# Kernel optimization log

Measured on AMD Instinct MI355X. Metric: run time of the kernel, lower is better.

Reference implementation:

```python
import jax, jax.numpy as jnp
import numpy as np
from jax import lax

HIDDEN = 256
HORIZON = 168  # 7 * 24


def _cell(x, h, c, Wih, Whh, bih, bhh):
    # PyTorch LSTM cell: gate order i, f, g, o
    gates = x @ Wih.T + bih + h @ Whh.T + bhh  # [B, 4*HIDDEN]
    i, f, g, o = jnp.split(gates, 4, axis=-1)
    c = jax.nn.sigmoid(f) * c + jax.nn.sigmoid(i) * jnp.tanh(g)
    h = jax.nn.sigmoid(o) * jnp.tanh(c)
    return h, c


def setup_inputs() -> dict:
    key = jax.random.key(0)
    ks = jax.random.split(key, 20)
    B, T, H = 1024, 336, HIDDEN
    s = 0.05

    def p(k, shape):
        return jax.random.normal(k, shape, dtype=jnp.float32) * s

    inp = {"x": jax.random.normal(ks[0], (B, T), dtype=jnp.float32)}
    # encoder layer 0 (input_size=1), layer 1 (input=HIDDEN)
    inp["enc_Wih0"] = p(ks[1], (4 * H, 1)); inp["enc_Whh0"] = p(ks[2], (4 * H, H))
    inp["enc_bih0"] = p(ks[3], (4 * H,)); inp["enc_bhh0"] = p(ks[4], (4 * H,))
    inp["enc_Wih1"] = p(ks[5], (4 * H, H)); inp["enc_Whh1"] = p(ks[6], (4 * H, H))
    inp["enc_bih1"] = p(ks[7], (4 * H,)); inp["enc_bhh1"] = p(ks[8], (4 * H,))
    # decoder layers
    inp["dec_Wih0"] = p(ks[9], (4 * H, 1)); inp["dec_Whh0"] = p(ks[10], (4 * H, H))
    inp["dec_bih0"] = p(ks[11], (4 * H,)); inp["dec_bhh0"] = p(ks[12], (4 * H,))
    inp["dec_Wih1"] = p(ks[13], (4 * H, H)); inp["dec_Whh1"] = p(ks[14], (4 * H, H))
    inp["dec_bih1"] = p(ks[15], (4 * H,)); inp["dec_bhh1"] = p(ks[16], (4 * H,))
    # final projection hidden -> 1
    inp["fc_W"] = p(ks[17], (1, H)); inp["fc_b"] = p(ks[18], (1,))
    return inp


def reference(x, enc_Wih0, enc_Whh0, enc_bih0, enc_bhh0,
              enc_Wih1, enc_Whh1, enc_bih1, enc_bhh1,
              dec_Wih0, dec_Whh0, dec_bih0, dec_bhh0,
              dec_Wih1, dec_Whh1, dec_bih1, dec_bhh1,
              fc_W, fc_b):
    B = x.shape[0]
    xs = x[:, :, None].transpose(1, 0, 2)  # [T, B, 1]
    z = jnp.zeros((B, HIDDEN), dtype=x.dtype)

    def enc_step(carry, xt):
        h0, c0, h1, c1 = carry
        h0, c0 = _cell(xt, h0, c0, enc_Wih0, enc_Whh0, enc_bih0, enc_bhh0)
        h1, c1 = _cell(h0, h1, c1, enc_Wih1, enc_Whh1, enc_bih1, enc_bhh1)
        return (h0, c0, h1, c1), None

    (h0, c0, h1, c1), _ = lax.scan(enc_step, (z, z, z, z), xs)

    dec_inp = x[:, -1:]  # [B, 1] last observed value

    def dec_step(carry, _):
        h0, c0, h1, c1, inp = carry
        h0, c0 = _cell(inp, h0, c0, dec_Wih0, dec_Whh0, dec_bih0, dec_bhh0)
        h1, c1 = _cell(h0, h1, c1, dec_Wih1, dec_Whh1, dec_bih1, dec_bhh1)
        pred = h1 @ fc_W.T + fc_b  # [B, 1]
        return (h0, c0, h1, c1, pred), pred

    _, preds = lax.scan(dec_step, (h0, c0, h1, c1, dec_inp), None, length=HORIZON)
    return preds[:, :, 0].T  # [B, HORIZON]
```

## Files before the change

kernel.cpp:

```cpp
#include <hip/hip_runtime.h>

#define HIDDEN 256
#define TENC 336
#define HORIZ 168
#define BSZ 1024
#define BH (BSZ*HIDDEN)

typedef _Float16 f16;
typedef f16 f16x8 __attribute__((ext_vector_type(8)));
typedef float f32x4 __attribute__((ext_vector_type(4)));
typedef unsigned int u32;
typedef unsigned long long u64;

#define H0_OFF 0
#define H1_OFF (2*BH*2)
#define PRED_OFF (H1_OFF + 2*BH*2)
#define FLAG_OFF (PRED_OFF + 2*BSZ*4)
#define WS_TOTAL (FLAG_OFF + 256*128)

#define LDS_A0 0
#define LDS_A1 32768
#define LDS_X0 65536
#define LDS_X1 81920
#define LDS_SM 98304
#define LDS_TOTAL (LDS_SM + 1024)

__device__ __forceinline__ float sigm(float x){ return 1.0f/(1.0f+__expf(-x)); }
__device__ __forceinline__ float tanh_f(float x){ return 2.0f/(1.0f+__expf(-2.0f*x)) - 1.0f; }

__device__ __forceinline__ u64 ald64(const f16* p){
  return __hip_atomic_load((const u64*)p, __ATOMIC_RELAXED, __HIP_MEMORY_SCOPE_AGENT);
}
__device__ __forceinline__ u32 ald32(const u32* p){
  return __hip_atomic_load(p, __ATOMIC_RELAXED, __HIP_MEMORY_SCOPE_AGENT);
}
__device__ __forceinline__ float aldf(const float* p){
  return __hip_atomic_load(p, __ATOMIC_RELAXED, __HIP_MEMORY_SCOPE_AGENT);
}
__device__ __forceinline__ void ast32(u32* p, u32 v){
  __hip_atomic_store(p, v, __ATOMIC_RELAXED, __HIP_MEMORY_SCOPE_AGENT);
}
__device__ __forceinline__ void astf(float* p, float v){
  __hip_atomic_store(p, v, __ATOMIC_RELAXED, __HIP_MEMORY_SCOPE_AGENT);
}

__device__ __forceinline__ f16x8 loadWfrag(const float* W, int grow, int k){
  const float* p = W + grow*HIDDEN + k;
  float4 lo = *(const float4*)p;
  float4 hi = *(const float4*)(p+4);
  f16x8 r;
  r[0]=(f16)lo.x; r[1]=(f16)lo.y; r[2]=(f16)lo.z; r[3]=(f16)lo.w;
  r[4]=(f16)hi.x; r[5]=(f16)hi.y; r[6]=(f16)hi.z; r[7]=(f16)hi.w;
  return r;
}

__device__ __forceinline__ void stage_tile(char* dst, const f16* src_base, int g, int tid){
  #pragma unroll
  for (int i=0;i<4;++i){
    int s = tid + 512*i;
    int l = s & 63, f = s >> 6;
    int kt = f >> 2, mt = f & 3;
    int row = g*64 + mt*16 + (l&15);
    int k = kt*32 + 8*(l>>4);
    const f16* src = src_base + row*HIDDEN + k;
    u64 a = ald64(src), b = ald64(src+4);
    *(u64*)(dst + s*16) = a;
    *(u64*)(dst + s*16 + 8) = b;
  }
}

__device__ __forceinline__ void cellpair(const float* X, const float* bs, const float* wih, float xr,
                                         int crow, int dp, float& ca, float& cb, float& hA, float& hB){
  float iA = X[(0*64+crow)*16+dp  ] + bs[dp]      + xr*wih[dp];
  float iB = X[(0*64+crow)*16+dp+1] + bs[dp+1]    + xr*wih[dp+1];
  float fA = X[(1*64+crow)*16+dp  ] + bs[16+dp]   + xr*wih[16+dp];
  float fB = X[(1*64+crow)*16+dp+1] + bs[16+dp+1] + xr*wih[16+dp+1];
  float gA = X[(2*64+crow)*16+dp  ] + bs[32+dp]   + xr*wih[32+dp];
  float gB = X[(2*64+crow)*16+dp+1] + bs[32+dp+1] + xr*wih[32+dp+1];
  float oA = X[(3*64+crow)*16+dp  ] + bs[48+dp]   + xr*wih[48+dp];
  float oB = X[(3*64+crow)*16+dp+1] + bs[48+dp+1] + xr*wih[48+dp+1];
  ca = sigm(fA)*ca + sigm(iA)*tanh_f(gA);
  cb = sigm(fB)*cb + sigm(iB)*tanh_f(gB);
  hA = sigm(oA)*tanh_f(ca);
  hB = sigm(oB)*tanh_f(cb);
}

__device__ __forceinline__ void storeh(f16* base, int rowg, int col, float hA, float hB){
  u32 pk = (u32)__builtin_bit_cast(unsigned short, (f16)hA)
         | ((u32)__builtin_bit_cast(unsigned short, (f16)hB) << 16);
  __hip_atomic_store((u32*)(base + rowg*HIDDEN + col), pk, __ATOMIC_RELAXED, __HIP_MEMORY_SCOPE_AGENT);
}

__device__ __forceinline__ void gbar(u32* flags, int g, int j, int lane, int tid, u32 ev){
  __syncthreads();
  if (tid == 0) ast32(&flags[(g*16 + j)*32], ev);
  const u32* sp = &flags[(g*16 + (lane&15))*32];
  bool done = false;
  for (int it = 0; it < (1<<16) && !done; ++it){
    u32 v = ald32(sp);
    done = (__all((int)(v >= ev)) != 0);
  }
}

struct P {
  const float *x;
  const float *eWih0,*eWhh0,*eBih0,*eBhh0,*eWih1,*eWhh1,*eBih1,*eBhh1;
  const float *dWih0,*dWhh0,*dBih0,*dBhh0,*dWih1,*dWhh1,*dBih1,*dBhh1;
  const float *fcW,*fcB;
  float* out;
  char* ws;
};

__global__ void initk(char* ws){
  u32* p = (u32*)ws;
  size_t total = (size_t)WS_TOTAL / 4;
  for (size_t k = (size_t)blockIdx.x*blockDim.x + threadIdx.x; k < total;
       k += (size_t)gridDim.x*blockDim.x) p[k] = 0u;
}

__global__ __launch_bounds__(512, 2) void lstm_main(P p){
  const int tid  = threadIdx.x;
  const int lane = tid & 63;
  const int w    = tid >> 6;
  const int n    = w & 3;
  const int mh   = w >> 2;
  const int blk  = blockIdx.x;
  const int g    = blk & 15;
  const int j    = blk >> 4;

  extern __shared__ __align__(16) char smem[];
  char*  A0 = smem + LDS_A0;
  char*  A1 = smem + LDS_A1;
  float* X0 = (float*)(smem + LDS_X0);
  float* X1 = (float*)(smem + LDS_X1);
  float* wih0s = (float*)(smem + LDS_SM);
  float* b0s   = wih0s + 64;
  float* b1s   = wih0s + 128;
  float* fcWs  = wih0s + 192;
  float* fcbs  = wih0s + 208;

  f16*   h0buf = (f16*)(p.ws + H0_OFF);
  f16*   h1buf = (f16*)(p.ws + H1_OFF);
  float* predb = (float*)(p.ws + PRED_OFF);
  u32*   flags = (u32*)(p.ws + FLAG_OFF);

  const int crow = tid >> 3;
  const int dp   = (tid & 7) * 2;
  const int rowg = g*64 + crow;
  const int cold = j*16 + dp;

  float c0a=0.f, c0b=0.f, c1a=0.f, c1b=0.f;

  if (tid < 64){
    int gt = tid >> 4, d = tid & 15;
    int grow = gt*256 + j*16 + d;
    wih0s[tid] = p.eWih0[grow];
    b0s[tid] = p.eBih0[grow] + p.eBhh0[grow];
    b1s[tid] = p.eBih1[grow] + p.eBhh1[grow];
  }
  if (tid < 16) fcWs[tid] = p.fcW[j*16 + tid];
  if (tid == 0) fcbs[0] = p.fcB[0];

  f16x8 B0[8], B1i[8], B1h[8];
  {
    int grow = n*256 + j*16 + (lane & 15);
    int kb = 8*(lane>>4);
    #pragma unroll
    for (int kt=0; kt<8; ++kt){
      B0[kt]  = loadWfrag(p.eWhh0, grow, kt*32 + kb);
      B1i[kt] = loadWfrag(p.eWih1, grow, kt*32 + kb);
      B1h[kt] = loadWfrag(p.eWhh1, grow, kt*32 + kb);
    }
  }
  __syncthreads();

  u32 ev = 0;

  for (int r = 0; r <= TENC; ++r){
    stage_tile(A0, h0buf + ((r+1)&1)*BH, g, tid);
    stage_tile(A1, h1buf + (r&1)*BH,     g, tid);
    __syncthreads();

    f32x4 acc0[2] = {{0.f,0.f,0.f,0.f},{0.f,0.f,0.f,0.f}};
    f32x4 acc1[2] = {{0.f,0.f,0.f,0.f},{0.f,0.f,0.f,0.f}};
    #pragma unroll
    for (int kt=0; kt<8; ++kt){
      #pragma unroll
      for (int m=0; m<2; ++m){
        f16x8 a = *(const f16x8*)(A0 + ((kt*4 + (mh*2+m))*64 + lane)*16);
        acc0[m] = __builtin_amdgcn_mfma_f32_16x16x32_f16(a, B0[kt],  acc0[m], 0,0,0);
        acc1[m] = __builtin_amdgcn_mfma_f32_16x16x32_f16(a, B1i[kt], acc1[m], 0,0,0);
      }
    }
    #pragma unroll
    for (int kt=0; kt<8; ++kt){
      #pragma unroll
      for (int m=0; m<2; ++m){
        f16x8 a = *(const f16x8*)(A1 + ((kt*4 + (mh*2+m))*64 + lane)*16);
        acc1[m] = __builtin_amdgcn_mfma_f32_16x16x32_f16(a, B1h[kt], acc1[m], 0,0,0);
      }
    }

    #pragma unroll
    for (int m=0; m<2; ++m){
      int rb = mh*32 + m*16 + 4*(lane>>4);
      #pragma unroll
      for (int q=0; q<4; ++q){
        X0[(n*64 + rb + q)*16 + (lane&15)] = acc0[m][q];
        X1[(n*64 + rb + q)*16 + (lane&15)] = acc1[m][q];
      }
    }
    __syncthreads();

    if (r < TENC){
      float xr = p.x[rowg*TENC + r];
      float hA, hB;
      cellpair(X0, b0s, wih0s, xr, crow, dp, c0a, c0b, hA, hB);
      storeh(h0buf + (r&1)*BH, rowg, cold, hA, hB);
    }
    if (r >= 1){
      float hA, hB;
      cellpair(X1, b1s, wih0s, 0.f, crow, dp, c1a, c1b, hA, hB);
      storeh(h1buf + ((r-1)&1)*BH, rowg, cold, hA, hB);
    }
    ++ev;
    gbar(flags, g, j, lane, tid, ev);
  }

  __syncthreads();
  if (tid < 64){
    int gt = tid >> 4, d = tid & 15;
    int grow = gt*256 + j*16 + d;
    wih0s[tid] = p.dWih0[grow];
    b0s[tid] = p.dBih0[grow] + p.dBhh0[grow];
    b1s[tid] = p.dBih1[grow] + p.dBhh1[grow];
  }
  {
    int grow = n*256 + j*16 + (lane & 15);
    int kb = 8*(lane>>4);
    #pragma unroll
    for (int kt=0; kt<8; ++kt){
      B0[kt]  = loadWfrag(p.dWhh0, grow, kt*32 + kb);
      B1i[kt] = loadWfrag(p.dWih1, grow, kt*32 + kb);
      B1h[kt] = loadWfrag(p.dWhh1, grow, kt*32 + kb);
    }
  }
  __syncthreads();

  for (int t = 0; t < HORIZ; ++t){
    stage_tile(A0, h0buf + ((t+1)&1)*BH, g, tid);
    __syncthreads();

    f32x4 acc0[2] = {{0.f,0.f,0.f,0.f},{0.f,0.f,0.f,0.f}};
    #pragma unroll
    for (int kt=0; kt<8; ++kt){
      #pragma unroll
      for (int m=0; m<2; ++m){
        f16x8 a = *(const f16x8*)(A0 + ((kt*4 + (mh*2+m))*64 + lane)*16);
        acc0[m] = __builtin_amdgcn_mfma_f32_16x16x32_f16(a, B0[kt], acc0[m], 0,0,0);
      }
    }
    #pragma unroll
    for (int m=0; m<2; ++m){
      int rb = mh*32 + m*16 + 4*(lane>>4);
      #pragma unroll
      for (int q=0; q<4; ++q) X0[(n*64 + rb + q)*16 + (lane&15)] = acc0[m][q];
    }
    __syncthreads();

    float inp = (t == 0) ? p.x[rowg*TENC + (TENC-1)]
                         : aldf(&predb[((t+1)&1)*BSZ + rowg]);
    {
      float hA, hB;
      cellpair(X0, b0s, wih0s, inp, crow, dp, c0a, c0b, hA, hB);
      storeh(h0buf + (t&1)*BH, rowg, cold, hA, hB);
    }
    if (t > 0 && j == 0 && (tid & 7) == 0) p.out[rowg*HORIZ + (t-1)] = inp;
    ++ev;
    gbar(flags, g, j, lane, tid, ev);

    stage_tile(A0, h0buf + (t&1)*BH,     g, tid);
    stage_tile(A1, h1buf + ((t+1)&1)*BH, g, tid);
    __syncthreads();

    f32x4 acc1[2] = {{0.f,0.f,0.f,0.f},{0.f,0.f,0.f,0.f}};
    #pragma unroll
    for (int kt=0; kt<8; ++kt){
      #pragma unroll
      for (int m=0; m<2; ++m){
        f16x8 a0 = *(const f16x8*)(A0 + ((kt*4 + (mh*2+m))*64 + lane)*16);
        acc1[m] = __builtin_amdgcn_mfma_f32_16x16x32_f16(a0, B1i[kt], acc1[m], 0,0,0);
        f16x8 a1 = *(const f16x8*)(A1 + ((kt*4 + (mh*2+m))*64 + lane)*16);
        acc1[m] = __builtin_amdgcn_mfma_f32_16x16x32_f16(a1, B1h[kt], acc1[m], 0,0,0);
      }
    }
    #pragma unroll
    for (int m=0; m<2; ++m){
      int rb = mh*32 + m*16 + 4*(lane>>4);
      #pragma unroll
      for (int q=0; q<4; ++q) X1[(n*64 + rb + q)*16 + (lane&15)] = acc1[m][q];
    }
    __syncthreads();

    {
      float hA, hB;
      cellpair(X1, b1s, wih0s, 0.f, crow, dp, c1a, c1b, hA, hB);
      storeh(h1buf + (t&1)*BH, rowg, cold, hA, hB);
      float pp = fcWs[dp]*hA + fcWs[dp+1]*hB;
      pp += __shfl_xor(pp, 1);
      pp += __shfl_xor(pp, 2);
      pp += __shfl_xor(pp, 4);
      if ((tid & 7) == 0){
        float v = pp + (j == 0 ? fcbs[0] : 0.f);
        __hip_atomic_fetch_add(&predb[(t&1)*BSZ + rowg], v,
                               __ATOMIC_RELAXED, __HIP_MEMORY_SCOPE_AGENT);
        if (j == 0) astf(&predb[((t+1)&1)*BSZ + rowg], 0.f);
      }
    }
    ++ev;
    gbar(flags, g, j, lane, tid, ev);
  }

  if (j == 0 && (tid & 7) == 0){
    float v = aldf(&predb[((HORIZ-1)&1)*BSZ + rowg]);
    p.out[rowg*HORIZ + (HORIZ-1)] = v;
  }
}

extern "C" void kernel_launch(void* const* d_in, const int* in_sizes, int n_in,
                              void* d_out, int out_size, void* d_ws, size_t ws_size,
                              hipStream_t stream) {
  (void)in_sizes; (void)n_in; (void)out_size;
  if (ws_size < (size_t)WS_TOTAL) return;

  P prm;
  prm.x     = (const float*)d_in[0];
  prm.eWih0 = (const float*)d_in[1];  prm.eWhh0 = (const float*)d_in[2];
  prm.eBih0 = (const float*)d_in[3];  prm.eBhh0 = (const float*)d_in[4];
  prm.eWih1 = (const float*)d_in[5];  prm.eWhh1 = (const float*)d_in[6];
  prm.eBih1 = (const float*)d_in[7];  prm.eBhh1 = (const float*)d_in[8];
  prm.dWih0 = (const float*)d_in[9];  prm.dWhh0 = (const float*)d_in[10];
  prm.dBih0 = (const float*)d_in[11]; prm.dBhh0 = (const float*)d_in[12];
  prm.dWih1 = (const float*)d_in[13]; prm.dWhh1 = (const float*)d_in[14];
  prm.dBih1 = (const float*)d_in[15]; prm.dBhh1 = (const float*)d_in[16];
  prm.fcW   = (const float*)d_in[17]; prm.fcB   = (const float*)d_in[18];
  prm.out   = (float*)d_out;
  prm.ws    = (char*)d_ws;

  hipLaunchKernelGGL(initk, dim3(512), dim3(256), 0, stream, (char*)d_ws);

  hipFuncSetAttribute((const void*)lstm_main,
                      hipFuncAttributeMaxDynamicSharedMemorySize, LDS_TOTAL);
  void* args[] = { &prm };
  hipLaunchCooperativeKernel((const void*)lstm_main, dim3(256), dim3(512),
                             args, LDS_TOTAL, stream);
}
```

Measured before the change: 4.216 ms.

## Restructure LSTM step sync with counter barrier and hoist decoder Whh1 GEMM

Replaces the per-block flag barrier with one atomic arrival counter per row group, polled by a single wavefront. Moves the decoder layer-1 recurrent GEMM (h1·Whh1) before the first barrier so only the Wih1 half stays on the critical path. Prediction partials are now written to per-column slots and reduced with shuffles, replacing float atomics and buffer zeroing. Tile staging now issues all global loads before any LDS stores, and the gate scratch uses a padded stride to reduce LDS bank conflicts. The risk is atomic contention on the shared counter, plus more registers held during staging.

```diff
diff --git a/kernel.cpp b/kernel.cpp
--- a/kernel.cpp
+++ b/kernel.cpp
@@ -14,33 +14,28 @@
 
 #define H0_OFF 0
 #define H1_OFF (2*BH*2)
-#define PRED_OFF (H1_OFF + 2*BH*2)
-#define FLAG_OFF (PRED_OFF + 2*BSZ*4)
-#define WS_TOTAL (FLAG_OFF + 256*128)
+#define PP_OFF (H1_OFF + 2*BH*2)
+#define CNT_OFF (PP_OFF + BSZ*16*4)
+#define WS_TOTAL (CNT_OFF + 16*128)
 
 #define LDS_A0 0
 #define LDS_A1 32768
 #define LDS_X0 65536
-#define LDS_X1 81920
-#define LDS_SM 98304
+#define XSTRIDE 18
+#define LDS_X1 (LDS_X0 + 256*XSTRIDE*4)
+#define LDS_SM (LDS_X1 + 256*XSTRIDE*4)
 #define LDS_TOTAL (LDS_SM + 1024)
 
 __device__ __forceinline__ float sigm(float x){ return 1.0f/(1.0f+__expf(-x)); }
 __device__ __forceinline__ float tanh_f(float x){ return 2.0f/(1.0f+__expf(-2.0f*x)) - 1.0f; }
 
-__device__ __forceinline__ u64 ald64(const f16* p){
+__device__ __forceinline__ u64 ald64(const void* p){
   return __hip_atomic_load((const u64*)p, __ATOMIC_RELAXED, __HIP_MEMORY_SCOPE_AGENT);
 }
 __device__ __forceinline__ u32 ald32(const u32* p){
   return __hip_atomic_load(p, __ATOMIC_RELAXED, __HIP_MEMORY_SCOPE_AGENT);
 }
-__device__ __forceinline__ float aldf(const float* p){
-  return __hip_atomic_load(p, __ATOMIC_RELAXED, __HIP_MEMORY_SCOPE_AGENT);
-}
 __device__ __forceinline__ void ast32(u32* p, u32 v){
-  __hip_atomic_store(p, v, __ATOMIC_RELAXED, __HIP_MEMORY_SCOPE_AGENT);
-}
-__device__ __forceinline__ void astf(float* p, float v){
   __hip_atomic_store(p, v, __ATOMIC_RELAXED, __HIP_MEMORY_SCOPE_AGENT);
 }
 
@@ -54,31 +49,65 @@
   return r;
 }
 
+__device__ __forceinline__ const f16* slot_src(const f16* base, int g, int s){
+  int l = s & 63, f = s >> 6;
+  int kt = f >> 2, mt = f & 3;
+  int row = g*64 + mt*16 + (l&15);
+  int k = kt*32 + 8*(l>>4);
+  return base + row*HIDDEN + k;
+}
+
 __device__ __forceinline__ void stage_tile(char* dst, const f16* src_base, int g, int tid){
+  u64 v[8];
+  #pragma unroll
+  for (int i=0;i<4;++i){
+    const f16* src = slot_src(src_base, g, tid + 512*i);
+    v[2*i]   = ald64(src);
+    v[2*i+1] = ald64(src+4);
+  }
   #pragma unroll
   for (int i=0;i<4;++i){
     int s = tid + 512*i;
-    int l = s & 63, f = s >> 6;
-    int kt = f >> 2, mt = f & 3;
-    int row = g*64 + mt*16 + (l&15);
-    int k = kt*32 + 8*(l>>4);
-    const f16* src = src_base + row*HIDDEN + k;
-    u64 a = ald64(src), b = ald64(src+4);
-    *(u64*)(dst + s*16) = a;
-    *(u64*)(dst + s*16 + 8) = b;
+    *(u64*)(dst + s*16)     = v[2*i];
+    *(u64*)(dst + s*16 + 8) = v[2*i+1];
+  }
+}
+
+__device__ __forceinline__ void stage2(char* dA, const f16* sA, char* dB, const f16* sB,
+                                       int g, int tid){
+  u64 va[8], vb[8];
+  #pragma unroll
+  for (int i=0;i<4;++i){
+    const f16* src = slot_src(sA, g, tid + 512*i);
+    va[2*i]   = ald64(src);
+    va[2*i+1] = ald64(src+4);
+  }
+  #pragma unroll
+  for (int i=0;i<4;++i){
+    const f16* src = slot_src(sB, g, tid + 512*i);
+    vb[2*i]   = ald64(src);
+    vb[2*i+1] = ald64(src+4);
+  }
+  #pragma unroll
+  for (int i=0;i<4;++i){
+    int s = tid + 512*i;
+    *(u64*)(dA + s*16)     = va[2*i];
+    *(u64*)(dA + s*16 + 8) = va[2*i+1];
+    *(u64*)(dB + s*16)     = vb[2*i];
+    *(u64*)(dB + s*16 + 8) = vb[2*i+1];
   }
 }
 
 __device__ __forceinline__ void cellpair(const float* X, const float* bs, const float* wih, float xr,
                                          int crow, int dp, float& ca, float& cb, float& hA, float& hB){
-  float iA = X[(0*64+crow)*16+dp  ] + bs[dp]      + xr*wih[dp];
-  float iB = X[(0*64+crow)*16+dp+1] + bs[dp+1]    + xr*wih[dp+1];
-  float fA = X[(1*64+crow)*16+dp  ] + bs[16+dp]   + xr*wih[16+dp];
-  float fB = X[(1*64+crow)*16+dp+1] + bs[16+dp+1] + xr*wih[16+dp+1];
-  float gA = X[(2*64+crow)*16+dp  ] + bs[32+dp]   + xr*wih[32+dp];
-  float gB = X[(2*64+crow)*16+dp+1] + bs[32+dp+1] + xr*wih[32+dp+1];
-  float oA = X[(3*64+crow)*16+dp  ] + bs[48+dp]   + xr*wih[48+dp];
-  float oB = X[(3*64+crow)*16+dp+1] + bs[48+dp+1] + xr*wih[48+dp+1];
+  float iA = X[(0*64+crow)*XSTRIDE+dp  ] + bs[dp]      + xr*wih[dp];
+  float iB = X[(0*64+crow)*XSTRIDE+dp+1] + bs[dp+1]    + xr*wih[dp+1];
+  float fA = X[(1*64+crow)*XSTRIDE+dp  ] + bs[16+dp]   + xr*wih[16+dp];
+  float fB = X[(1*64+crow)*XSTRIDE+dp+1] + bs[16+dp+1] + xr*wih[16+dp+1];
+  float gA = X[(2*64+crow)*XSTRIDE+dp  ] + bs[32+dp]   + xr*wih[32+dp];
+  float gB = X[(2*64+crow)*XSTRIDE+dp+1] + bs[32+dp+1] + xr*wih[32+dp+1];
+  float oA = X[(3*64+crow)*XSTRIDE+dp  ] + bs[48+dp]   + xr*wih[48+dp];
+  float oB = X[(3*64+crow)*XSTRIDE+dp+1] + bs[48+dp+1] + xr*wih[48+dp+1];
   ca = sigm(fA)*ca + sigm(iA)*tanh_f(gA);
   cb = sigm(fB)*cb + sigm(iB)*tanh_f(gB);
   hA = sigm(oA)*tanh_f(ca);
@@ -88,18 +117,19 @@
 __device__ __forceinline__ void storeh(f16* base, int rowg, int col, float hA, float hB){
   u32 pk = (u32)__builtin_bit_cast(unsigned short, (f16)hA)
          | ((u32)__builtin_bit_cast(unsigned short, (f16)hB) << 16);
-  __hip_atomic_store((u32*)(base + rowg*HIDDEN + col), pk, __ATOMIC_RELAXED, __HIP_MEMORY_SCOPE_AGENT);
-}
-
-__device__ __forceinline__ void gbar(u32* flags, int g, int j, int lane, int tid, u32 ev){
+  ast32((u32*)(base + rowg*HIDDEN + col), pk);
+}
+
+__device__ __forceinline__ void gbar(u32* cnt, int tid, u32 target){
   __syncthreads();
-  if (tid == 0) ast32(&flags[(g*16 + j)*32], ev);
-  const u32* sp = &flags[(g*16 + (lane&15))*32];
-  bool done = false;
-  for (int it = 0; it < (1<<16) && !done; ++it){
-    u32 v = ald32(sp);
-    done = (__all((int)(v >= ev)) != 0);
-  }
+  if (tid == 0)
+    (void)__hip_atomic_fetch_add(cnt, 1u, __ATOMIC_RELAXED, __HIP_MEMORY_SCOPE_AGENT);
+  if (tid < 64){
+    for (int it = 0; it < (1<<17); ++it){
+      if (ald32(cnt) >= target) break;
+    }
+  }
+  __syncthreads();
 }
 
 struct P {
@@ -141,8 +171,8 @@
 
   f16*   h0buf = (f16*)(p.ws + H0_OFF);
   f16*   h1buf = (f16*)(p.ws + H1_OFF);
-  float* predb = (float*)(p.ws + PRED_OFF);
-  u32*   flags = (u32*)(p.ws + FLAG_OFF);
+  float* ppart = (float*)(p.ws + PP_OFF);
+  u32*   cnt   = (u32*)(p.ws + CNT_OFF) + g*32;
 
   const int crow = tid >> 3;
   const int dp   = (tid & 7) * 2;
@@ -177,8 +207,8 @@
   u32 ev = 0;
 
   for (int r = 0; r <= TENC; ++r){
-    stage_tile(A0, h0buf + ((r+1)&1)*BH, g, tid);
-    stage_tile(A1, h1buf + (r&1)*BH,     g, tid);
+    float xr = (r < TENC) ? p.x[rowg*TENC + r] : 0.f;
+    stage2(A0, h0buf + ((r+1)&1)*BH, A1, h1buf + (r&1)*BH, g, tid);
     __syncthreads();
 
     f32x4 acc0[2] = {{0.f,0.f,0.f,0.f},{0.f,0.f,0.f,0.f}};
@@ -206,14 +236,13 @@
       int rb = mh*32 + m*16 + 4*(lane>>4);
       #pragma unroll
       for (int q=0; q<4; ++q){
-        X0[(n*64 + rb + q)*16 + (lane&15)] = acc0[m][q];
-        X1[(n*64 + rb + q)*16 + (lane&15)] = acc1[m][q];
+        X0[(n*64 + rb + q)*XSTRIDE + (lane&15)] = acc0[m][q];
+        X1[(n*64 + rb + q)*XSTRIDE + (lane&15)] = acc1[m][q];
       }
     }
     __syncthreads();
 
     if (r < TENC){
-      float xr = p.x[rowg*TENC + r];
       float hA, hB;
       cellpair(X0, b0s, wih0s, xr, crow, dp, c0a, c0b, hA, hB);
       storeh(h0buf + (r&1)*BH, rowg, cold, hA, hB);
@@ -224,7 +253,7 @@
       storeh(h1buf + ((r-1)&1)*BH, rowg, cold, hA, hB);
     }
     ++ev;
-    gbar(flags, g, j, lane, tid, ev);
+    gbar(cnt, tid, 16u*ev);
   }
 
   __syncthreads();
@@ -248,28 +277,46 @@
   __syncthreads();
 
   for (int t = 0; t < HORIZ; ++t){
-    stage_tile(A0, h0buf + ((t+1)&1)*BH, g, tid);
+    u64 ppv = 0;
+    float xlast = 0.f;
+    if (t == 0) xlast = p.x[rowg*TENC + (TENC-1)];
+    else        ppv   = ald64(ppart + rowg*16 + (tid&7)*2);
+
+    stage2(A0, h0buf + ((t+1)&1)*BH, A1, h1buf + ((t+1)&1)*BH, g, tid);
     __syncthreads();
 
     f32x4 acc0[2] = {{0.f,0.f,0.f,0.f},{0.f,0.f,0.f,0.f}};
+    f32x4 acc1[2] = {{0.f,0.f,0.f,0.f},{0.f,0.f,0.f,0.f}};
     #pragma unroll
     for (int kt=0; kt<8; ++kt){
       #pragma unroll
       for (int m=0; m<2; ++m){
-        f16x8 a = *(const f16x8*)(A0 + ((kt*4 + (mh*2+m))*64 + lane)*16);
-        acc0[m] = __builtin_amdgcn_mfma_f32_16x16x32_f16(a, B0[kt], acc0[m], 0,0,0);
+        f16x8 a0 = *(const f16x8*)(A0 + ((kt*4 + (mh*2+m))*64 + lane)*16);
+        acc0[m] = __builtin_amdgcn_mfma_f32_16x16x32_f16(a0, B0[kt],  acc0[m], 0,0,0);
+        f16x8 a1 = *(const f16x8*)(A1 + ((kt*4 + (mh*2+m))*64 + lane)*16);
+        acc1[m] = __builtin_amdgcn_mfma_f32_16x16x32_f16(a1, B1h[kt], acc1[m], 0,0,0);
       }
     }
     #pragma unroll
     for (int m=0; m<2; ++m){
       int rb = mh*32 + m*16 + 4*(lane>>4);
       #pragma unroll
-      for (int q=0; q<4; ++q) X0[(n*64 + rb + q)*16 + (lane&15)] = acc0[m][q];
-    }
-    __syncthreads();
-
-    float inp = (t == 0) ? p.x[rowg*TENC + (TENC-1)]
-                         : aldf(&predb[((t+1)&1)*BSZ + rowg]);
+      for (int q=0; q<4; ++q) X0[(n*64 + rb + q)*XSTRIDE + (lane&15)] = acc0[m][q];
+    }
+    __syncthreads();
+
+    float inp;
+    if (t == 0){
+      inp = xlast;
+    } else {
+      float a = __builtin_bit_cast(float, (u32)(ppv & 0xffffffffull));
+      float b = __builtin_bit_cast(float, (u32)(ppv >> 32));
+      float s = a + b;
+      s += __shfl_xor(s, 1);
+      s += __shfl_xor(s, 2);
+      s += __shfl_xor(s, 4);
+      inp = s + fcbs[0];
+    }
     {
       float hA, hB;
       cellpair(X0, b0s, wih0s, inp, crow, dp, c0a, c0b, hA, hB);
@@ -277,28 +324,24 @@
     }
     if (t > 0 && j == 0 && (tid & 7) == 0) p.out[rowg*HORIZ + (t-1)] = inp;
     ++ev;
-    gbar(flags, g, j, lane, tid, ev);
-
-    stage_tile(A0, h0buf + (t&1)*BH,     g, tid);
-    stage_tile(A1, h1buf + ((t+1)&1)*BH, g, tid);
-    __syncthreads();
-
-    f32x4 acc1[2] = {{0.f,0.f,0.f,0.f},{0.f,0.f,0.f,0.f}};
+    gbar(cnt, tid, 16u*ev);
+
+    stage_tile(A0, h0buf + (t&1)*BH, g, tid);
+    __syncthreads();
+
     #pragma unroll
     for (int kt=0; kt<8; ++kt){
       #pragma unroll
       for (int m=0; m<2; ++m){
         f16x8 a0 = *(const f16x8*)(A0 + ((kt*4 + (mh*2+m))*64 + lane)*16);
         acc1[m] = __builtin_amdgcn_mfma_f32_16x16x32_f16(a0, B1i[kt], acc1[m], 0,0,0);
-        f16x8 a1 = *(const f16x8*)(A1 + ((kt*4 + (mh*2+m))*64 + lane)*16);
-        acc1[m] = __builtin_amdgcn_mfma_f32_16x16x32_f16(a1, B1h[kt], acc1[m], 0,0,0);
       }
     }
     #pragma unroll
     for (int m=0; m<2; ++m){
       int rb = mh*32 + m*16 + 4*(lane>>4);
       #pragma unroll
-      for (int q=0; q<4; ++q) X1[(n*64 + rb + q)*16 + (lane&15)] = acc1[m][q];
+      for (int q=0; q<4; ++q) X1[(n*64 + rb + q)*XSTRIDE + (lane&15)] = acc1[m][q];
     }
     __syncthreads();
 
@@ -310,20 +353,22 @@
       pp += __shfl_xor(pp, 1);
       pp += __shfl_xor(pp, 2);
       pp += __shfl_xor(pp, 4);
-      if ((tid & 7) == 0){
-        float v = pp + (j == 0 ? fcbs[0] : 0.f);
-        __hip_atomic_fetch_add(&predb[(t&1)*BSZ + rowg], v,
-                               __ATOMIC_RELAXED, __HIP_MEMORY_SCOPE_AGENT);
-        if (j == 0) astf(&predb[((t+1)&1)*BSZ + rowg], 0.f);
-      }
+      if ((tid & 7) == 0)
+        ast32((u32*)(ppart + rowg*16 + j), __builtin_bit_cast(u32, pp));
     }
     ++ev;
-    gbar(flags, g, j, lane, tid, ev);
-  }
-
-  if (j == 0 && (tid & 7) == 0){
-    float v = aldf(&predb[((HORIZ-1)&1)*BSZ + rowg]);
-    p.out[rowg*HORIZ + (HORIZ-1)] = v;
+    gbar(cnt, tid, 16u*ev);
+  }
+
+  if (j == 0){
+    u64 ppv = ald64(ppart + rowg*16 + (tid&7)*2);
+    float a = __builtin_bit_cast(float, (u32)(ppv & 0xffffffffull));
+    float b = __builtin_bit_cast(float, (u32)(ppv >> 32));
+    float s = a + b;
+    s += __shfl_xor(s, 1);
+    s += __shfl_xor(s, 2);
+    s += __shfl_xor(s, 4);
+    if ((tid & 7) == 0) p.out[rowg*HORIZ + (HORIZ-1)] = s + fcbs[0];
   }
 }
 
```

New measurement: 4.034 ms. 4.3% less time.

## Split LSTM layers into concurrent wave chains with per-wave flag synchronization

Applied to the files above, without the earlier changes.

Each block now runs the two LSTM layers on separate groups of waves (chain 0 for layer 0, chain 1 for layer 1), so layer 0 can run ahead of layer 1 in a wavefront pipeline. The block-wide global barriers are replaced by per-wave flag polling against only the producer slices each wave needs. A triple-buffered h0 gives the slack for that. Hidden state is stored in a pre-swizzled MFMA fragment layout and loaded straight into registers, so the LDS staging disappears. The prediction reduction moves from float atomics to per-slice partial sums. This removes full-barrier latency on the serial recurrence, at the cost of more registers (launch bounds drop to one block per CU) and more complex fine-grained polling.

```diff
diff --git a/kernel.cpp b/kernel.cpp
--- a/kernel.cpp
+++ b/kernel.cpp
@@ -13,22 +13,16 @@
 typedef unsigned long long u64;
 
 #define H0_OFF 0
-#define H1_OFF (2*BH*2)
-#define PRED_OFF (H1_OFF + 2*BH*2)
-#define FLAG_OFF (PRED_OFF + 2*BSZ*4)
-#define WS_TOTAL (FLAG_OFF + 256*128)
-
-#define LDS_A0 0
-#define LDS_A1 32768
-#define LDS_X0 65536
-#define LDS_X1 81920
-#define LDS_SM 98304
-#define LDS_TOTAL (LDS_SM + 1024)
+#define H1_OFF (3*BH*2)
+#define PP_OFF (H1_OFF + 2*BH*2)
+#define F0_OFF (PP_OFF + 2*BSZ*16*4)
+#define F1_OFF (F0_OFF + 1024*64)
+#define WS_TOTAL (F1_OFF + 1024*64)
 
 __device__ __forceinline__ float sigm(float x){ return 1.0f/(1.0f+__expf(-x)); }
 __device__ __forceinline__ float tanh_f(float x){ return 2.0f/(1.0f+__expf(-2.0f*x)) - 1.0f; }
 
-__device__ __forceinline__ u64 ald64(const f16* p){
+__device__ __forceinline__ u64 ald64(const void* p){
   return __hip_atomic_load((const u64*)p, __ATOMIC_RELAXED, __HIP_MEMORY_SCOPE_AGENT);
 }
 __device__ __forceinline__ u32 ald32(const u32* p){
@@ -38,9 +32,6 @@
   return __hip_atomic_load(p, __ATOMIC_RELAXED, __HIP_MEMORY_SCOPE_AGENT);
 }
 __device__ __forceinline__ void ast32(u32* p, u32 v){
-  __hip_atomic_store(p, v, __ATOMIC_RELAXED, __HIP_MEMORY_SCOPE_AGENT);
-}
-__device__ __forceinline__ void astf(float* p, float v){
   __hip_atomic_store(p, v, __ATOMIC_RELAXED, __HIP_MEMORY_SCOPE_AGENT);
 }
 
@@ -54,51 +45,74 @@
   return r;
 }
 
-__device__ __forceinline__ void stage_tile(char* dst, const f16* src_base, int g, int tid){
-  #pragma unroll
-  for (int i=0;i<4;++i){
-    int s = tid + 512*i;
-    int l = s & 63, f = s >> 6;
-    int kt = f >> 2, mt = f & 3;
-    int row = g*64 + mt*16 + (l&15);
-    int k = kt*32 + 8*(l>>4);
-    const f16* src = src_base + row*HIDDEN + k;
-    u64 a = ald64(src), b = ald64(src+4);
-    *(u64*)(dst + s*16) = a;
-    *(u64*)(dst + s*16 + 8) = b;
-  }
-}
-
-__device__ __forceinline__ void cellpair(const float* X, const float* bs, const float* wih, float xr,
-                                         int crow, int dp, float& ca, float& cb, float& hA, float& hB){
-  float iA = X[(0*64+crow)*16+dp  ] + bs[dp]      + xr*wih[dp];
-  float iB = X[(0*64+crow)*16+dp+1] + bs[dp+1]    + xr*wih[dp+1];
-  float fA = X[(1*64+crow)*16+dp  ] + bs[16+dp]   + xr*wih[16+dp];
-  float fB = X[(1*64+crow)*16+dp+1] + bs[16+dp+1] + xr*wih[16+dp+1];
-  float gA = X[(2*64+crow)*16+dp  ] + bs[32+dp]   + xr*wih[32+dp];
-  float gB = X[(2*64+crow)*16+dp+1] + bs[32+dp+1] + xr*wih[32+dp+1];
-  float oA = X[(3*64+crow)*16+dp  ] + bs[48+dp]   + xr*wih[48+dp];
-  float oB = X[(3*64+crow)*16+dp+1] + bs[48+dp+1] + xr*wih[48+dp+1];
-  ca = sigm(fA)*ca + sigm(iA)*tanh_f(gA);
-  cb = sigm(fB)*cb + sigm(iB)*tanh_f(gB);
-  hA = sigm(oA)*tanh_f(ca);
-  hB = sigm(oB)*tanh_f(cb);
-}
-
-__device__ __forceinline__ void storeh(f16* base, int rowg, int col, float hA, float hB){
-  u32 pk = (u32)__builtin_bit_cast(unsigned short, (f16)hA)
-         | ((u32)__builtin_bit_cast(unsigned short, (f16)hB) << 16);
-  __hip_atomic_store((u32*)(base + rowg*HIDDEN + col), pk, __ATOMIC_RELAXED, __HIP_MEMORY_SCOPE_AGENT);
-}
-
-__device__ __forceinline__ void gbar(u32* flags, int g, int j, int lane, int tid, u32 ev){
-  __syncthreads();
-  if (tid == 0) ast32(&flags[(g*16 + j)*32], ev);
-  const u32* sp = &flags[(g*16 + (lane&15))*32];
-  bool done = false;
-  for (int it = 0; it < (1<<16) && !done; ++it){
-    u32 v = ald32(sp);
-    done = (__all((int)(v >= ev)) != 0);
+__device__ __forceinline__ void pollw2(const u32* f0, u32 t0, const u32* f1, u32 t1, int lane){
+  const u32* sp = nullptr; u32 tgt = 0;
+  if (lane < 16){ sp = f0 + lane*64; tgt = t0; }
+  else if (f1 != nullptr && lane < 32){ sp = f1 + (lane-16)*64; tgt = t1; }
+  for (int it = 0; it < (1<<20); ++it){
+    bool ok = (sp == nullptr) || (ald32(sp) >= tgt);
+    if (__all((int)ok)) break;
+  }
+}
+
+__device__ __forceinline__ void sigw(u32* line, u32 v, int lane){
+  asm volatile("s_waitcnt vmcnt(0)" ::: "memory");
+  if (lane == 0) ast32(line, v);
+}
+
+__device__ __forceinline__ void loadA8(f16x8* a, const f16* ub, int lane){
+  #pragma unroll
+  for (int kt=0; kt<8; ++kt){
+    const f16* q = ub + kt*512 + lane*8;
+    union { u64 w[2]; f16x8 v; } u;
+    u.w[0] = ald64(q); u.w[1] = ald64(q+4);
+    a[kt] = u.v;
+  }
+}
+
+__device__ __forceinline__ void mm4(f32x4* acc, const f16x8* a, const f16x8 B[4][8]){
+  #pragma unroll
+  for (int kt=0; kt<8; ++kt){
+    #pragma unroll
+    for (int n=0; n<4; ++n)
+      acc[n] = __builtin_amdgcn_mfma_f32_16x16x32_f16(a[kt], B[n][kt], acc[n], 0,0,0);
+  }
+}
+__device__ __forceinline__ void mm4l(f32x4* acc, const f16x8* a, const char* WL, int lane){
+  #pragma unroll
+  for (int kt=0; kt<8; ++kt){
+    #pragma unroll
+    for (int n=0; n<4; ++n){
+      f16x8 bf = *(const f16x8*)(WL + ((n*8+kt)*64 + lane)*16);
+      acc[n] = __builtin_amdgcn_mfma_f32_16x16x32_f16(a[kt], bf, acc[n], 0,0,0);
+    }
+  }
+}
+
+__device__ __forceinline__ void cell4(const f32x4* acc, const float* b, const float* wx,
+                                      const float* x4, float* c, float* h4){
+  #pragma unroll
+  for (int q=0; q<4; ++q){
+    float pi = acc[0][q] + b[0] + x4[q]*wx[0];
+    float pf = acc[1][q] + b[1] + x4[q]*wx[1];
+    float pg = acc[2][q] + b[2] + x4[q]*wx[2];
+    float po = acc[3][q] + b[3] + x4[q]*wx[3];
+    float i = sigm(pi), f = sigm(pf), gg = tanh_f(pg), o = sigm(po);
+    c[q] = f*c[q] + i*gg;
+    h4[q] = o*tanh_f(c[q]);
+  }
+}
+
+__device__ __forceinline__ void storeH(f16* slotbase, int unit, int hi, int d, int D, const float* h4){
+  #pragma unroll
+  for (int q=0; q<4; ++q){
+    float ph = __shfl_xor(h4[q], 1);
+    if (!(d & 1)){
+      u32 pk = (u32)__builtin_bit_cast(unsigned short, (f16)h4[q])
+             | ((u32)__builtin_bit_cast(unsigned short, (f16)ph) << 16);
+      f16* ad = slotbase + unit*4096 + (D>>5)*512 + ((hi*4+q) + 16*((D&31)>>3))*8 + (D&7);
+      ast32((u32*)ad, pk);
+    }
   }
 }
 
@@ -118,212 +132,188 @@
        k += (size_t)gridDim.x*blockDim.x) p[k] = 0u;
 }
 
-__global__ __launch_bounds__(512, 2) void lstm_main(P p){
+__global__ __launch_bounds__(512) void lstm_main(P p){
   const int tid  = threadIdx.x;
   const int lane = tid & 63;
   const int w    = tid >> 6;
-  const int n    = w & 3;
-  const int mh   = w >> 2;
-  const int blk  = blockIdx.x;
-  const int g    = blk & 15;
-  const int j    = blk >> 4;
-
-  extern __shared__ __align__(16) char smem[];
-  char*  A0 = smem + LDS_A0;
-  char*  A1 = smem + LDS_A1;
-  float* X0 = (float*)(smem + LDS_X0);
-  float* X1 = (float*)(smem + LDS_X1);
-  float* wih0s = (float*)(smem + LDS_SM);
-  float* b0s   = wih0s + 64;
-  float* b1s   = wih0s + 128;
-  float* fcWs  = wih0s + 192;
-  float* fcbs  = wih0s + 208;
+  const int chain= w >> 2;
+  const int v    = w & 3;
+  const int g    = blockIdx.x & 15;
+  const int j    = blockIdx.x >> 4;
+  const int hi   = lane >> 4;
+  const int d    = lane & 15;
+  const int D    = j*16 + d;
+  const int unit = g*4 + v;
+
+  __shared__ __align__(16) char sWL[32768];
 
   f16*   h0buf = (f16*)(p.ws + H0_OFF);
   f16*   h1buf = (f16*)(p.ws + H1_OFF);
-  float* predb = (float*)(p.ws + PRED_OFF);
-  u32*   flags = (u32*)(p.ws + FLAG_OFF);
-
-  const int crow = tid >> 3;
-  const int dp   = (tid & 7) * 2;
-  const int rowg = g*64 + crow;
-  const int cold = j*16 + dp;
-
-  float c0a=0.f, c0b=0.f, c1a=0.f, c1b=0.f;
-
-  if (tid < 64){
-    int gt = tid >> 4, d = tid & 15;
-    int grow = gt*256 + j*16 + d;
-    wih0s[tid] = p.eWih0[grow];
-    b0s[tid] = p.eBih0[grow] + p.eBhh0[grow];
-    b1s[tid] = p.eBih1[grow] + p.eBhh1[grow];
-  }
-  if (tid < 16) fcWs[tid] = p.fcW[j*16 + tid];
-  if (tid == 0) fcbs[0] = p.fcB[0];
-
-  f16x8 B0[8], B1i[8], B1h[8];
-  {
-    int grow = n*256 + j*16 + (lane & 15);
-    int kb = 8*(lane>>4);
-    #pragma unroll
-    for (int kt=0; kt<8; ++kt){
-      B0[kt]  = loadWfrag(p.eWhh0, grow, kt*32 + kb);
-      B1i[kt] = loadWfrag(p.eWih1, grow, kt*32 + kb);
-      B1h[kt] = loadWfrag(p.eWhh1, grow, kt*32 + kb);
-    }
+  float* ppart = (float*)(p.ws + PP_OFF);
+  u32*   F0    = (u32*)(p.ws + F0_OFF);
+  u32*   F1    = (u32*)(p.ws + F1_OFF);
+  const u32* pF0 = F0 + ((g*16 + 0)*4 + v)*16;
+  const u32* pF1 = F1 + ((g*16 + 0)*4 + v)*16;
+  u32* myF0 = F0 + ((g*16 + j)*4 + v)*16;
+  u32* myF1 = F1 + ((g*16 + j)*4 + v)*16;
+
+  int rows[4];
+  #pragma unroll
+  for (int q=0; q<4; ++q) rows[q] = g*64 + v*16 + hi*4 + q;
+
+  f16x8 B[4][8];
+  float c[4] = {0.f,0.f,0.f,0.f};
+  float wx[4], b0[4];
+  float fcw = 0.f, fcb = 0.f;
+
+  if (chain == 0){
+    #pragma unroll
+    for (int n=0; n<4; ++n){
+      #pragma unroll
+      for (int kt=0; kt<8; ++kt)
+        B[n][kt] = loadWfrag(p.eWhh0, n*256 + j*16 + d, kt*32 + 8*hi);
+      wx[n] = p.eWih0[n*256 + D];
+      b0[n] = p.eBih0[n*256 + D] + p.eBhh0[n*256 + D];
+    }
+  } else {
+    #pragma unroll
+    for (int n=0; n<4; ++n){
+      #pragma unroll
+      for (int kt=0; kt<8; ++kt)
+        B[n][kt] = loadWfrag(p.eWih1, n*256 + j*16 + d, kt*32 + 8*hi);
+      wx[n] = 0.f;
+      b0[n] = p.eBih1[n*256 + D] + p.eBhh1[n*256 + D];
+    }
+    #pragma unroll
+    for (int kt=0; kt<8; ++kt)
+      *(f16x8*)(sWL + ((v*8+kt)*64 + lane)*16) =
+        loadWfrag(p.eWhh1, v*256 + j*16 + d, kt*32 + 8*hi);
   }
   __syncthreads();
 
-  u32 ev = 0;
-
-  for (int r = 0; r <= TENC; ++r){
-    stage_tile(A0, h0buf + ((r+1)&1)*BH, g, tid);
-    stage_tile(A1, h1buf + (r&1)*BH,     g, tid);
-    __syncthreads();
-
-    f32x4 acc0[2] = {{0.f,0.f,0.f,0.f},{0.f,0.f,0.f,0.f}};
-    f32x4 acc1[2] = {{0.f,0.f,0.f,0.f},{0.f,0.f,0.f,0.f}};
-    #pragma unroll
-    for (int kt=0; kt<8; ++kt){
-      #pragma unroll
-      for (int m=0; m<2; ++m){
-        f16x8 a = *(const f16x8*)(A0 + ((kt*4 + (mh*2+m))*64 + lane)*16);
-        acc0[m] = __builtin_amdgcn_mfma_f32_16x16x32_f16(a, B0[kt],  acc0[m], 0,0,0);
-        acc1[m] = __builtin_amdgcn_mfma_f32_16x16x32_f16(a, B1i[kt], acc1[m], 0,0,0);
-      }
-    }
-    #pragma unroll
-    for (int kt=0; kt<8; ++kt){
-      #pragma unroll
-      for (int m=0; m<2; ++m){
-        f16x8 a = *(const f16x8*)(A1 + ((kt*4 + (mh*2+m))*64 + lane)*16);
-        acc1[m] = __builtin_amdgcn_mfma_f32_16x16x32_f16(a, B1h[kt], acc1[m], 0,0,0);
-      }
-    }
-
-    #pragma unroll
-    for (int m=0; m<2; ++m){
-      int rb = mh*32 + m*16 + 4*(lane>>4);
+  if (chain == 0){
+    for (int r = 0; r < TENC; ++r){
+      float x4[4];
+      #pragma unroll
+      for (int q=0; q<4; ++q) x4[q] = p.x[rows[q]*TENC + r];
+      pollw2(pF0, (u32)r, pF1, (r>=2)?(u32)(r-2):0u, lane);
+      f16x8 a[8];
+      loadA8(a, h0buf + ((r+2)%3)*BH + unit*4096, lane);
+      f32x4 acc[4] = {{0,0,0,0},{0,0,0,0},{0,0,0,0},{0,0,0,0}};
+      mm4(acc, a, B);
+      float h4[4];
+      cell4(acc, b0, wx, x4, c, h4);
+      storeH(h0buf + (r%3)*BH, unit, hi, d, D, h4);
+      sigw(myF0, (u32)(r+1), lane);
+    }
+  } else {
+    for (int r = 0; r < TENC; ++r){
+      pollw2(pF0, (u32)(r+1), pF1, (u32)r, lane);
+      f16x8 a0[8], a1[8];
+      loadA8(a0, h0buf + (r%3)*BH + unit*4096, lane);
+      loadA8(a1, h1buf + ((r+1)&1)*BH + unit*4096, lane);
+      f32x4 acc[4] = {{0,0,0,0},{0,0,0,0},{0,0,0,0},{0,0,0,0}};
+      mm4(acc, a0, B);
+      mm4l(acc, a1, sWL, lane);
+      float h4[4], xz[4] = {0.f,0.f,0.f,0.f};
+      cell4(acc, b0, wx, xz, c, h4);
+      storeH(h1buf + (r&1)*BH, unit, hi, d, D, h4);
+      sigw(myF1, (u32)(r+1), lane);
+    }
+  }
+
+  __syncthreads();
+  if (chain == 0){
+    #pragma unroll
+    for (int n=0; n<4; ++n){
+      #pragma unroll
+      for (int kt=0; kt<8; ++kt)
+        B[n][kt] = loadWfrag(p.dWhh0, n*256 + j*16 + d, kt*32 + 8*hi);
+      wx[n] = p.dWih0[n*256 + D];
+      b0[n] = p.dBih0[n*256 + D] + p.dBhh0[n*256 + D];
+    }
+    fcb = p.fcB[0];
+  } else {
+    #pragma unroll
+    for (int n=0; n<4; ++n){
+      #pragma unroll
+      for (int kt=0; kt<8; ++kt)
+        B[n][kt] = loadWfrag(p.dWih1, n*256 + j*16 + d, kt*32 + 8*hi);
+      b0[n] = p.dBih1[n*256 + D] + p.dBhh1[n*256 + D];
+    }
+    #pragma unroll
+    for (int kt=0; kt<8; ++kt)
+      *(f16x8*)(sWL + ((v*8+kt)*64 + lane)*16) =
+        loadWfrag(p.dWhh1, v*256 + j*16 + d, kt*32 + 8*hi);
+    fcw = p.fcW[D];
+  }
+  __syncthreads();
+
+  if (chain == 0){
+    for (int t = 0; t < HORIZ; ++t){
+      float inp4[4];
+      if (t == 0){
+        #pragma unroll
+        for (int q=0; q<4; ++q) inp4[q] = p.x[rows[q]*TENC + (TENC-1)];
+      }
+      pollw2(pF0, (u32)(336+t), pF1, (t==0)?335u:(u32)(336+t), lane);
+      if (t > 0){
+        float pp4[4];
+        #pragma unroll
+        for (int q=0; q<4; ++q) pp4[q] = aldf(ppart + ((t-1)&1)*BSZ*16 + rows[q]*16 + d);
+        #pragma unroll
+        for (int q=0; q<4; ++q){
+          float s = pp4[q];
+          s += __shfl_xor(s, 1); s += __shfl_xor(s, 2);
+          s += __shfl_xor(s, 4); s += __shfl_xor(s, 8);
+          inp4[q] = s + fcb;
+        }
+      }
+      f16x8 a[8];
+      loadA8(a, h0buf + ((335+t)%3)*BH + unit*4096, lane);
+      f32x4 acc[4] = {{0,0,0,0},{0,0,0,0},{0,0,0,0},{0,0,0,0}};
+      mm4(acc, a, B);
+      float h4[4];
+      cell4(acc, b0, wx, inp4, c, h4);
+      storeH(h0buf + ((336+t)%3)*BH, unit, hi, d, D, h4);
+      if (t > 0 && j == 0 && d == 0){
+        #pragma unroll
+        for (int q=0; q<4; ++q) p.out[rows[q]*HORIZ + (t-1)] = inp4[q];
+      }
+      sigw(myF0, (u32)(337+t), lane);
+    }
+    if (j == 0){
+      pollw2(pF1, 504u, nullptr, 0, lane);
       #pragma unroll
       for (int q=0; q<4; ++q){
-        X0[(n*64 + rb + q)*16 + (lane&15)] = acc0[m][q];
-        X1[(n*64 + rb + q)*16 + (lane&15)] = acc1[m][q];
-      }
-    }
-    __syncthreads();
-
-    if (r < TENC){
-      float xr = p.x[rowg*TENC + r];
-      float hA, hB;
-      cellpair(X0, b0s, wih0s, xr, crow, dp, c0a, c0b, hA, hB);
-      storeh(h0buf + (r&1)*BH, rowg, cold, hA, hB);
-    }
-    if (r >= 1){
-      float hA, hB;
-      cellpair(X1, b1s, wih0s, 0.f, crow, dp, c1a, c1b, hA, hB);
-      storeh(h1buf + ((r-1)&1)*BH, rowg, cold, hA, hB);
-    }
-    ++ev;
-    gbar(flags, g, j, lane, tid, ev);
-  }
-
-  __syncthreads();
-  if (tid < 64){
-    int gt = tid >> 4, d = tid & 15;
-    int grow = gt*256 + j*16 + d;
-    wih0s[tid] = p.dWih0[grow];
-    b0s[tid] = p.dBih0[grow] + p.dBhh0[grow];
-    b1s[tid] = p.dBih1[grow] + p.dBhh1[grow];
-  }
-  {
-    int grow = n*256 + j*16 + (lane & 15);
-    int kb = 8*(lane>>4);
-    #pragma unroll
-    for (int kt=0; kt<8; ++kt){
-      B0[kt]  = loadWfrag(p.dWhh0, grow, kt*32 + kb);
-      B1i[kt] = loadWfrag(p.dWih1, grow, kt*32 + kb);
-      B1h[kt] = loadWfrag(p.dWhh1, grow, kt*32 + kb);
-    }
-  }
-  __syncthreads();
-
-  for (int t = 0; t < HORIZ; ++t){
-    stage_tile(A0, h0buf + ((t+1)&1)*BH, g, tid);
-    __syncthreads();
-
-    f32x4 acc0[2] = {{0.f,0.f,0.f,0.f},{0.f,0.f,0.f,0.f}};
-    #pragma unroll
-    for (int kt=0; kt<8; ++kt){
-      #pragma unroll
-      for (int m=0; m<2; ++m){
-        f16x8 a = *(const f16x8*)(A0 + ((kt*4 + (mh*2+m))*64 + lane)*16);
-        acc0[m] = __builtin_amdgcn_mfma_f32_16x16x32_f16(a, B0[kt], acc0[m], 0,0,0);
-      }
-    }
-    #pragma unroll
-    for (int m=0; m<2; ++m){
-      int rb = mh*32 + m*16 + 4*(lane>>4);
-      #pragma unroll
-      for (int q=0; q<4; ++q) X0[(n*64 + rb + q)*16 + (lane&15)] = acc0[m][q];
-    }
-    __syncthreads();
-
-    float inp = (t == 0) ? p.x[rowg*TENC + (TENC-1)]
-                         : aldf(&predb[((t+1)&1)*BSZ + rowg]);
-    {
-      float hA, hB;
-      cellpair(X0, b0s, wih0s, inp, crow, dp, c0a, c0b, hA, hB);
-      storeh(h0buf + (t&1)*BH, rowg, cold, hA, hB);
-    }
-    if (t > 0 && j == 0 && (tid & 7) == 0) p.out[rowg*HORIZ + (t-1)] = inp;
-    ++ev;
-    gbar(flags, g, j, lane, tid, ev);
-
-    stage_tile(A0, h0buf + (t&1)*BH,     g, tid);
-    stage_tile(A1, h1buf + ((t+1)&1)*BH, g, tid);
-    __syncthreads();
-
-    f32x4 acc1[2] = {{0.f,0.f,0.f,0.f},{0.f,0.f,0.f,0.f}};
-    #pragma unroll
-    for (int kt=0; kt<8; ++kt){
-      #pragma unroll
-      for (int m=0; m<2; ++m){
-        f16x8 a0 = *(const f16x8*)(A0 + ((kt*4 + (mh*2+m))*64 + lane)*16);
-        acc1[m] = __builtin_amdgcn_mfma_f32_16x16x32_f16(a0, B1i[kt], acc1[m], 0,0,0);
-        f16x8 a1 = *(const f16x8*)(A1 + ((kt*4 + (mh*2+m))*64 + lane)*16);
-        acc1[m] = __builtin_amdgcn_mfma_f32_16x16x32_f16(a1, B1h[kt], acc1[m], 0,0,0);
-      }
-    }
-    #pragma unroll
-    for (int m=0; m<2; ++m){
-      int rb = mh*32 + m*16 + 4*(lane>>4);
-      #pragma unroll
-      for (int q=0; q<4; ++q) X1[(n*64 + rb + q)*16 + (lane&15)] = acc1[m][q];
-    }
-    __syncthreads();
-
-    {
-      float hA, hB;
-      cellpair(X1, b1s, wih0s, 0.f, crow, dp, c1a, c1b, hA, hB);
-      storeh(h1buf + (t&1)*BH, rowg, cold, hA, hB);
-      float pp = fcWs[dp]*hA + fcWs[dp+1]*hB;
-      pp += __shfl_xor(pp, 1);
-      pp += __shfl_xor(pp, 2);
-      pp += __shfl_xor(pp, 4);
-      if ((tid & 7) == 0){
-        float v = pp + (j == 0 ? fcbs[0] : 0.f);
-        __hip_atomic_fetch_add(&predb[(t&1)*BSZ + rowg], v,
-                               __ATOMIC_RELAXED, __HIP_MEMORY_SCOPE_AGENT);
-        if (j == 0) astf(&predb[((t+1)&1)*BSZ + rowg], 0.f);
-      }
-    }
-    ++ev;
-    gbar(flags, g, j, lane, tid, ev);
-  }
-
-  if (j == 0 && (tid & 7) == 0){
-    float v = aldf(&predb[((HORIZ-1)&1)*BSZ + rowg]);
-    p.out[rowg*HORIZ + (HORIZ-1)] = v;
+        float s = aldf(ppart + (167&1)*BSZ*16 + rows[q]*16 + d);
+        s += __shfl_xor(s, 1); s += __shfl_xor(s, 2);
+        s += __shfl_xor(s, 4); s += __shfl_xor(s, 8);
+        if (d == 0) p.out[rows[q]*HORIZ + (HORIZ-1)] = s + fcb;
+      }
+    }
+  } else {
+    for (int t = 0; t < HORIZ; ++t){
+      pollw2(pF0, (u32)(337+t), pF1, (u32)(336+t), lane);
+      f16x8 a0[8], a1[8];
+      loadA8(a0, h0buf + ((336+t)%3)*BH + unit*4096, lane);
+      loadA8(a1, h1buf + ((t+1)&1)*BH + unit*4096, lane);
+      f32x4 acc[4] = {{0,0,0,0},{0,0,0,0},{0,0,0,0},{0,0,0,0}};
+      mm4(acc, a0, B);
+      mm4l(acc, a1, sWL, lane);
+      float h4[4], xz[4] = {0.f,0.f,0.f,0.f};
+      cell4(acc, b0, wx, xz, c, h4);
+      storeH(h1buf + (t&1)*BH, unit, hi, d, D, h4);
+      #pragma unroll
+      for (int q=0; q<4; ++q){
+        float s = fcw * h4[q];
+        s += __shfl_xor(s, 1); s += __shfl_xor(s, 2);
+        s += __shfl_xor(s, 4); s += __shfl_xor(s, 8);
+        if (d == 0)
+          ast32((u32*)(ppart + (t&1)*BSZ*16 + rows[q]*16 + j), __builtin_bit_cast(u32, s));
+      }
+      sigw(myF1, (u32)(337+t), lane);
+    }
   }
 }
 
@@ -347,11 +337,9 @@
   prm.out   = (float*)d_out;
   prm.ws    = (char*)d_ws;
 
-  hipLaunchKernelGGL(initk, dim3(512), dim3(256), 0, stream, (char*)d_ws);
-
-  hipFuncSetAttribute((const void*)lstm_main,
-                      hipFuncAttributeMaxDynamicSharedMemorySize, LDS_TOTAL);
+  hipLaunchKernelGGL(initk, dim3(256), dim3(256), 0, stream, (char*)d_ws);
+
   void* args[] = { &prm };
   hipLaunchCooperativeKernel((const void*)lstm_main, dim3(256), dim3(512),
-                             args, LDS_TOTAL, stream);
-}
+                             args, 0, stream);
+}
```

New measurement: 4.325 ms. 2.6% more time.
